# Optimization experiments

Measured on AMD Instinct MI355X. Metric: run time of the kernel, lower is better.

The kernel has to match this reference:

```python
import jax, jax.numpy as jnp
import numpy as np

B, S, D, H = 4, 2048, 1024, 16
HD = D // H  # head dim = 64


def setup_inputs() -> dict:
    key = jax.random.key(0)
    ks = jax.random.split(key, 5)
    scale = 0.02
    return {
        "x": jax.random.normal(ks[0], (B, S, D), dtype=jnp.float32),
        "w_qkv": jax.random.normal(ks[1], (D, 3 * D), dtype=jnp.float32) * scale,
        "b_qkv": jax.random.normal(ks[2], (3 * D,), dtype=jnp.float32) * scale,
        "w_proj": jax.random.normal(ks[3], (D, D), dtype=jnp.float32) * scale,
        "b_proj": jax.random.normal(ks[4], (D,), dtype=jnp.float32) * scale,
    }


def reference(x, w_qkv, b_qkv, w_proj, b_proj):
    # Fused QKV projection: [B,S,D] @ [D,3D] -> [B,S,3D]
    qkv = jnp.einsum('bsd,de->bse', x, w_qkv) + b_qkv
    q, k, v = jnp.split(qkv, 3, axis=-1)
    # [B,S,D] -> [B,H,S,hd]
    def heads(t):
        return t.reshape(B, S, H, HD).transpose(0, 2, 1, 3)
    q, k, v = heads(q), heads(k), heads(v)
    # Scaled dot-product attention (non-causal, matching torch SDPA defaults)
    scores = jnp.einsum('bhsd,bhtd->bhst', q, k) / jnp.sqrt(jnp.float32(HD))
    attn = jax.nn.softmax(scores, axis=-1)
    out = jnp.einsum('bhst,bhtd->bhsd', attn, v)
    # [B,H,S,hd] -> [B,S,D]
    out = out.transpose(0, 2, 1, 3).reshape(B, S, D)
    return jnp.einsum('bsd,de->bse', out, w_proj) + b_proj
```

## Files before the change

kernel.cpp:

```cpp
#include <hip/hip_runtime.h>
#include <hip/hip_bf16.h>
#include <cstdint>

typedef __attribute__((ext_vector_type(8))) __bf16 bf16x8;
typedef __attribute__((ext_vector_type(4))) __bf16 bf16x4;
typedef __attribute__((ext_vector_type(4))) float f32x4;

#define MFMA16(a, b, c) __builtin_amdgcn_mfma_f32_16x16x32_bf16(a, b, c, 0, 0, 0)

static constexpr float SCQ = 0.18033688f;

__device__ __forceinline__ void gload16(const void* g, void* l) {
  __builtin_amdgcn_global_load_lds(
      (const __attribute__((address_space(1))) void*)g,
      (__attribute__((address_space(3))) void*)l, 16, 0, 0);
}

__global__ __launch_bounds__(256) void conv_x(const float* __restrict__ in,
                                              __bf16* __restrict__ out) {
  const size_t i = ((size_t)blockIdx.x * 256 + threadIdx.x) * 8;
  const float4 v0 = *(const float4*)(in + i);
  const float4 v1 = *(const float4*)(in + i + 4);
  bf16x8 o = {(__bf16)v0.x, (__bf16)v0.y, (__bf16)v0.z, (__bf16)v0.w,
              (__bf16)v1.x, (__bf16)v1.y, (__bf16)v1.z, (__bf16)v1.w};
  *(bf16x8*)(out + i) = o;
}

__global__ __launch_bounds__(256) void conv_wt(const float* __restrict__ W,
                                               __bf16* __restrict__ Wt,
                                               int K, int N) {
  __shared__ float tile[64][65];
  const int nb = blockIdx.x * 64, kb = blockIdx.y * 64;
  const int t = threadIdx.x, tr = t >> 4, tc = t & 15;
  #pragma unroll
  for (int p = 0; p < 4; ++p) {
    const float4 v =
        *(const float4*)(W + (size_t)(kb + p * 16 + tr) * N + nb + tc * 4);
    tile[p * 16 + tr][tc * 4 + 0] = v.x;
    tile[p * 16 + tr][tc * 4 + 1] = v.y;
    tile[p * 16 + tr][tc * 4 + 2] = v.z;
    tile[p * 16 + tr][tc * 4 + 3] = v.w;
  }
  __syncthreads();
  #pragma unroll
  for (int p = 0; p < 4; ++p) {
    const int n = p * 16 + tr, kk = tc * 4;
    bf16x4 o = {(__bf16)tile[kk + 0][n], (__bf16)tile[kk + 1][n],
                (__bf16)tile[kk + 2][n], (__bf16)tile[kk + 3][n]};
    *(bf16x4*)(Wt + (size_t)(nb + n) * K + kb + kk) = o;
  }
}

__global__ __launch_bounds__(256) void qkv_gemm_b(
    const __bf16* __restrict__ A, const __bf16* __restrict__ Bt,
    const float* __restrict__ bias,
    __bf16* __restrict__ Qb, __bf16* __restrict__ Kb, __bf16* __restrict__ Vt)
{
  __shared__ alignas(16) __bf16 a_sh[128 * 32];
  __shared__ alignas(16) __bf16 b_sh[128 * 32];
  const int id = blockIdx.x;
  const int wg = (id & 7) * 192 + (id >> 3);
  const int n0 = (wg % 24) * 128, m0 = (wg / 24) * 128;
  const int t = threadIdx.x, wave = t >> 6, lane = t & 63;
  const int r = lane & 15, g = lane >> 4;
  const int wm = (wave >> 1) * 64, wn = (wave & 1) * 64;
  f32x4 acc[4][4] = {};

  const int srow = wave * 16 + (lane >> 2);
  const int scol = (lane & 3) * 8;
  const __bf16* gA = A + (size_t)(m0 + srow) * 1024 + scol;
  const __bf16* gB = Bt + (size_t)(n0 + srow) * 1024 + scol;
  __bf16* lA = a_sh + wave * 512;
  __bf16* lB = b_sh + wave * 512;

  for (int k0 = 0; k0 < 1024; k0 += 32) {
    __syncthreads();
    gload16(gA + k0, lA);
    gload16(gA + 64 * 1024 + k0, lA + 2048);
    gload16(gB + k0, lB);
    gload16(gB + 64 * 1024 + k0, lB + 2048);
    __syncthreads();
    bf16x8 af[4], bfr[4];
    #pragma unroll
    for (int i = 0; i < 4; ++i)
      af[i] = *(bf16x8*)&a_sh[(wm + i * 16 + r) * 32 + g * 8];
    #pragma unroll
    for (int j = 0; j < 4; ++j)
      bfr[j] = *(bf16x8*)&b_sh[(wn + j * 16 + r) * 32 + g * 8];
    #pragma unroll
    for (int i = 0; i < 4; ++i)
      #pragma unroll
      for (int j = 0; j < 4; ++j)
        acc[i][j] = MFMA16(af[i], bfr[j], acc[i][j]);
  }

  const int which = n0 >> 10;
  const int bb = m0 >> 11;
  const int sbase = (m0 & 2047) + wm;
  #pragma unroll
  for (int j = 0; j < 4; ++j) {
    const int nc = n0 + wn + j * 16 + r;
    const float bv = bias[nc];
    const int hh = (nc & 1023) >> 6;
    const int d = nc & 63;
    #pragma unroll
    for (int i = 0; i < 4; ++i) {
      const int ss0 = sbase + i * 16 + g * 4;
      if (which == 0) {
        #pragma unroll
        for (int rr = 0; rr < 4; ++rr)
          Qb[((size_t)(bb * 16 + hh) * 2048 + ss0 + rr) * 64 + d] =
              (__bf16)((acc[i][j][rr] + bv) * SCQ);
      } else if (which == 1) {
        #pragma unroll
        for (int rr = 0; rr < 4; ++rr)
          Kb[((size_t)(bb * 16 + hh) * 2048 + ss0 + rr) * 64 +
             (d ^ ((((ss0 + rr) & 7)) << 3))] =
              (__bf16)(acc[i][j][rr] + bv);
      } else {
        bf16x4 vv;
        #pragma unroll
        for (int rr = 0; rr < 4; ++rr) vv[rr] = (__bf16)(acc[i][j][rr] + bv);
        const int v5 = ss0 & 31;
        const int pcol = (ss0 & ~31) + 8 * ((v5 >> 2) & 3) + 4 * (v5 >> 4);
        const int scol2 = (pcol & ~127) | ((pcol & 127) ^ ((d & 7) << 3));
        *(bf16x4*)&Vt[((size_t)(bb * 16 + hh) * 64 + d) * 2048 + scol2] = vv;
      }
    }
  }
}

__global__ __launch_bounds__(256) void proj_gemm_b(
    const __bf16* __restrict__ A, const __bf16* __restrict__ Bt,
    const float* __restrict__ bias, float* __restrict__ out)
{
  __shared__ alignas(16) __bf16 a_sh[128 * 32];
  __shared__ alignas(16) __bf16 b_sh[128 * 32];
  const int id = blockIdx.x;
  const int wg = (id & 7) * 64 + (id >> 3);
  const int n0 = (wg & 7) * 128, m0 = (wg >> 3) * 128;
  const int t = threadIdx.x, wave = t >> 6, lane = t & 63;
  const int r = lane & 15, g = lane >> 4;
  const int wm = (wave >> 1) * 64, wn = (wave & 1) * 64;
  f32x4 acc[4][4] = {};

  const int srow = wave * 16 + (lane >> 2);
  const int scol = (lane & 3) * 8;
  const __bf16* gA = A + (size_t)(m0 + srow) * 1024 + scol;
  const __bf16* gB = Bt + (size_t)(n0 + srow) * 1024 + scol;
  __bf16* lA = a_sh + wave * 512;
  __bf16* lB = b_sh + wave * 512;

  for (int k0 = 0; k0 < 1024; k0 += 32) {
    __syncthreads();
    gload16(gA + k0, lA);
    gload16(gA + 64 * 1024 + k0, lA + 2048);
    gload16(gB + k0, lB);
    gload16(gB + 64 * 1024 + k0, lB + 2048);
    __syncthreads();
    bf16x8 af[4], bfr[4];
    #pragma unroll
    for (int i = 0; i < 4; ++i)
      af[i] = *(bf16x8*)&a_sh[(wm + i * 16 + r) * 32 + g * 8];
    #pragma unroll
    for (int j = 0; j < 4; ++j)
      bfr[j] = *(bf16x8*)&b_sh[(wn + j * 16 + r) * 32 + g * 8];
    #pragma unroll
    for (int i = 0; i < 4; ++i)
      #pragma unroll
      for (int j = 0; j < 4; ++j)
        acc[i][j] = MFMA16(af[i], bfr[j], acc[i][j]);
  }

  #pragma unroll
  for (int j = 0; j < 4; ++j) {
    const int nc = n0 + wn + j * 16 + r;
    const float bv = bias[nc];
    #pragma unroll
    for (int i = 0; i < 4; ++i)
      #pragma unroll
      for (int rr = 0; rr < 4; ++rr)
        out[(size_t)(m0 + wm + i * 16 + g * 4 + rr) * 1024 + nc] =
            acc[i][j][rr] + bv;
  }
}

__global__ __launch_bounds__(256, 4) void attn_kernel(
    const __bf16* __restrict__ Q, const __bf16* __restrict__ K,
    const __bf16* __restrict__ Vt, __bf16* __restrict__ AO)
{
  __shared__ alignas(16) char lds[2][16384];

  const int p = blockIdx.x;
  const int hd = (p & 7) + 8 * (p >> 7);
  const int qt = (p >> 3) & 15;
  const int b = hd >> 4, h = hd & 15;

  const int t = threadIdx.x, wave = t >> 6, lane = t & 63;
  const int r = lane & 15, g = lane >> 4;

  const __bf16* Qp = Q + (size_t)hd * (2048 * 64);
  const char* Kh = (const char*)(K + (size_t)hd * (2048 * 64));
  const char* Vh = (const char*)(Vt + (size_t)hd * (64 * 2048));
  const int q0 = qt * 128 + wave * 32;

  bf16x8 qf[2][2];
  #pragma unroll
  for (int qh = 0; qh < 2; ++qh)
    #pragma unroll
    for (int hh = 0; hh < 2; ++hh)
      qf[qh][hh] =
          *(const bf16x8*)(Qp + (size_t)(q0 + qh * 16 + r) * 64 + hh * 32 + g * 8);

  float mrun[2] = {0.f, 0.f};
  float lrun[2] = {0.f, 0.f};
  f32x4 o[4][2] = {};

  const int lofs0 = wave * 1024;
  const int gofs0 = wave * 1024 + lane * 16;

  #define STAGE(t32, bi)                                                  \
    {                                                                     \
      char* lb = lds[bi];                                                 \
      _Pragma("unroll")                                                   \
      for (int rnd = 0; rnd < 2; ++rnd) {                                 \
        const int fb = rnd * 4096 + gofs0;                                \
        gload16(Kh + (size_t)(t32) * 8192 + fb, lb + rnd * 4096 + lofs0); \
        gload16(Vh + (size_t)(fb >> 7) * 4096 + (size_t)(t32) * 128 +     \
                    (fb & 127),                                           \
                lb + 8192 + rnd * 4096 + lofs0);                          \
      }                                                                   \
    }

  STAGE(0, 0);
  __syncthreads();

  const int sw = (r & 7) << 4;

  for (int t32 = 0; t32 < 32; ++t32) {
    const int cur = t32 & 1;
    if (t32 < 31) STAGE(t32 + 1, cur ^ 1);

    const char* kb = lds[cur];
    const char* vb = lds[cur] + 8192;

    f32x4 sacc[4][2];
    const f32x4 seed0 = {-mrun[0], -mrun[0], -mrun[0], -mrun[0]};
    const f32x4 seed1 = {-mrun[1], -mrun[1], -mrun[1], -mrun[1]};
    __builtin_amdgcn_s_setprio(1);
    #pragma unroll
    for (int kt = 0; kt < 4; ++kt) {
      const int rowb = (kt * 16 + r) * 128;
      const bf16x8 kf0 = *(const bf16x8*)(kb + rowb + ((16 * g) ^ sw));
      const bf16x8 kf1 = *(const bf16x8*)(kb + rowb + ((64 + 16 * g) ^ sw));
      f32x4 s0 = MFMA16(kf0, qf[0][0], seed0);
      s0 = MFMA16(kf1, qf[0][1], s0);
      sacc[kt][0] = s0;
      f32x4 s1 = MFMA16(kf0, qf[1][0], seed1);
      s1 = MFMA16(kf1, qf[1][1], s1);
      sacc[kt][1] = s1;
    }
    __builtin_amdgcn_s_setprio(0);

    bf16x8 pf[2][2];
    #pragma unroll
    for (int qh = 0; qh < 2; ++qh) {
      float a0 = fmaxf(fmaxf(sacc[0][qh][0], sacc[0][qh][1]),
                       fmaxf(sacc[0][qh][2], sacc[0][qh][3]));
      float a1 = fmaxf(fmaxf(sacc[1][qh][0], sacc[1][qh][1]),
                       fmaxf(sacc[1][qh][2], sacc[1][qh][3]));
      float a2 = fmaxf(fmaxf(sacc[2][qh][0], sacc[2][qh][1]),
                       fmaxf(sacc[2][qh][2], sacc[2][qh][3]));
      float a3 = fmaxf(fmaxf(sacc[3][qh][0], sacc[3][qh][1]),
                       fmaxf(sacc[3][qh][2], sacc[3][qh][3]));
      const float tm = fmaxf(fmaxf(a0, a1), fmaxf(a2, a3));

      float s = 0.f;
      if (__any(tm > 6.0f)) {
        float rm = fmaxf(tm, __shfl_xor(tm, 16));
        rm = fmaxf(rm, __shfl_xor(rm, 32));
        const float dl = fmaxf(rm, 0.f);
        const float al = exp2f(-dl);
        mrun[qh] += dl;
        #pragma unroll
        for (int kt = 0; kt < 4; ++kt)
          #pragma unroll
          for (int rr = 0; rr < 4; ++rr) {
            const float e = exp2f(sacc[kt][qh][rr] - dl);
            s += e;
            pf[qh][kt >> 1][(kt & 1) * 4 + rr] = (__bf16)e;
          }
        lrun[qh] = lrun[qh] * al + s;
        #pragma unroll
        for (int dt = 0; dt < 4; ++dt)
          #pragma unroll
          for (int rr = 0; rr < 4; ++rr)
            o[dt][qh][rr] *= al;
      } else {
        #pragma unroll
        for (int kt = 0; kt < 4; ++kt)
          #pragma unroll
          for (int rr = 0; rr < 4; ++rr) {
            const float e = exp2f(sacc[kt][qh][rr]);
            s += e;
            pf[qh][kt >> 1][(kt & 1) * 4 + rr] = (__bf16)e;
          }
        lrun[qh] += s;
      }
    }

    __builtin_amdgcn_s_setprio(1);
    #pragma unroll
    for (int c = 0; c < 2; ++c)
      #pragma unroll
      for (int dt = 0; dt < 4; ++dt) {
        const bf16x8 vf = *(const bf16x8*)(vb + (dt * 16 + r) * 128 +
                                           ((c * 64 + 16 * g) ^ sw));
        o[dt][0] = MFMA16(vf, pf[0][c], o[dt][0]);
        o[dt][1] = MFMA16(vf, pf[1][c], o[dt][1]);
      }
    __builtin_amdgcn_s_setprio(0);

    __syncthreads();
  }
  #undef STAGE

  #pragma unroll
  for (int qh = 0; qh < 2; ++qh) {
    float lr = lrun[qh];
    lr += __shfl_xor(lr, 16);
    lr += __shfl_xor(lr, 32);
    const float inv = 1.0f / lr;
    const int ss = q0 + qh * 16 + r;
    #pragma unroll
    for (int dt = 0; dt < 4; ++dt) {
      bf16x4 ov;
      #pragma unroll
      for (int rr = 0; rr < 4; ++rr)
        ov[rr] = (__bf16)(o[dt][qh][rr] * inv);
      *(bf16x4*)&AO[((size_t)b * 2048 + ss) * 1024 + h * 64 + dt * 16 + 4 * g] = ov;
    }
  }
}

extern "C" void kernel_launch(void* const* d_in, const int* in_sizes, int n_in,
                              void* d_out, int out_size, void* d_ws, size_t ws_size,
                              hipStream_t stream) {
  (void)in_sizes; (void)n_in; (void)out_size; (void)ws_size;
  const float* x      = (const float*)d_in[0];
  const float* w_qkv  = (const float*)d_in[1];
  const float* b_qkv  = (const float*)d_in[2];
  const float* w_proj = (const float*)d_in[3];
  const float* b_proj = (const float*)d_in[4];
  float* out = (float*)d_out;

  char* ws = (char*)d_ws;
  const size_t E2 = (size_t)8192 * 1024 * 2;
  __bf16* Qb  = (__bf16*)(ws);
  __bf16* Kb  = (__bf16*)(ws + E2);
  __bf16* Vt  = (__bf16*)(ws + 2 * E2);
  __bf16* Xb  = (__bf16*)(ws + 3 * E2);
  __bf16* AO  = Xb;
  __bf16* Wqt = (__bf16*)(ws + 4 * E2);
  __bf16* Wpt = (__bf16*)(ws + 4 * E2 + (size_t)3072 * 1024 * 2);

  conv_x<<<4096, 256, 0, stream>>>(x, Xb);
  conv_wt<<<dim3(48, 16), 256, 0, stream>>>(w_qkv, Wqt, 1024, 3072);
  conv_wt<<<dim3(16, 16), 256, 0, stream>>>(w_proj, Wpt, 1024, 1024);
  qkv_gemm_b<<<1536, 256, 0, stream>>>(Xb, Wqt, b_qkv, Qb, Kb, Vt);
  attn_kernel<<<1024, 256, 0, stream>>>(Qb, Kb, Vt, AO);
  proj_gemm_b<<<512, 256, 0, stream>>>(AO, Wpt, b_proj, out);
}
```

Before: 245.6 us.

## Replace GEMMs with 128x256-tile, 8-wave, triple-buffered pipelined kernel

The two separate QKV and projection GEMM kernels become one templated kernel that uses 128x256 tiles, 512 threads and a K-step of 64. Global-to-LDS loads are triple-buffered with prefetch two steps ahead, and a XOR swizzle avoids LDS bank conflicts. MFMA phases are split with s_setprio and explicit barriers so memory latency overlaps with compute. The large LDS footprint (144KB) limits occupancy to one block per CU, and the projection grid shrinks to 256 blocks, which may underfill the GPU.

Result: no change. 241.3 us (-1.8%).

```diff
diff --git a/kernel.cpp b/kernel.cpp
--- a/kernel.cpp
+++ b/kernel.cpp
@@ -51,137 +51,170 @@
   }
 }
 
-__global__ __launch_bounds__(256) void qkv_gemm_b(
+template <int MODE>
+__global__ __launch_bounds__(512) void gemm_t4(
     const __bf16* __restrict__ A, const __bf16* __restrict__ Bt,
     const float* __restrict__ bias,
-    __bf16* __restrict__ Qb, __bf16* __restrict__ Kb, __bf16* __restrict__ Vt)
+    __bf16* __restrict__ Qb, __bf16* __restrict__ Kb, __bf16* __restrict__ Vt,
+    float* __restrict__ outF)
 {
-  __shared__ alignas(16) __bf16 a_sh[128 * 32];
-  __shared__ alignas(16) __bf16 b_sh[128 * 32];
+  __shared__ alignas(16) char lds_[3 * 49152];
+
   const int id = blockIdx.x;
-  const int wg = (id & 7) * 192 + (id >> 3);
-  const int n0 = (wg % 24) * 128, m0 = (wg / 24) * 128;
-  const int t = threadIdx.x, wave = t >> 6, lane = t & 63;
+  constexpr int NB = (MODE == 0) ? 12 : 4;
+  constexpr int CH = (MODE == 0) ? 96 : 32;
+  const int wg = (id & 7) * CH + (id >> 3);
+  const int m0 = (wg / NB) * 128;
+  const int n0 = (wg % NB) * 256;
+
+  const int t = threadIdx.x, w = t >> 6, lane = t & 63;
   const int r = lane & 15, g = lane >> 4;
-  const int wm = (wave >> 1) * 64, wn = (wave & 1) * 64;
+  const int wr = w >> 2, wc = w & 3;
+
+  const char* Ac = (const char*)A + (size_t)m0 * 2048;
+  const char* Bc = (const char*)Bt + (size_t)n0 * 2048;
+
+  #define STAGE(kt_)                                                       \
+    {                                                                      \
+      char* lb = lds_ + ((kt_) % 3) * 49152;                               \
+      _Pragma("unroll")                                                    \
+      for (int rnd = 0; rnd < 2; ++rnd) {                                  \
+        const int c = rnd * 512 + t;                                       \
+        const int row = c >> 3;                                            \
+        const int kc = (c & 7) ^ (row & 7);                                \
+        gload16(Ac + (size_t)row * 2048 + (kt_) * 128 + kc * 16,           \
+                lb + rnd * 8192 + t * 16);                                 \
+      }                                                                    \
+      _Pragma("unroll")                                                    \
+      for (int rnd = 0; rnd < 4; ++rnd) {                                  \
+        const int c = rnd * 512 + t;                                       \
+        const int row = c >> 3;                                            \
+        const int kc = (c & 7) ^ (row & 7);                                \
+        gload16(Bc + (size_t)row * 2048 + (kt_) * 128 + kc * 16,           \
+                lb + 16384 + rnd * 8192 + t * 16);                         \
+      }                                                                    \
+    }
+
   f32x4 acc[4][4] = {};
-
-  const int srow = wave * 16 + (lane >> 2);
-  const int scol = (lane & 3) * 8;
-  const __bf16* gA = A + (size_t)(m0 + srow) * 1024 + scol;
-  const __bf16* gB = Bt + (size_t)(n0 + srow) * 1024 + scol;
-  __bf16* lA = a_sh + wave * 512;
-  __bf16* lB = b_sh + wave * 512;
-
-  for (int k0 = 0; k0 < 1024; k0 += 32) {
-    __syncthreads();
-    gload16(gA + k0, lA);
-    gload16(gA + 64 * 1024 + k0, lA + 2048);
-    gload16(gB + k0, lB);
-    gload16(gB + 64 * 1024 + k0, lB + 2048);
-    __syncthreads();
-    bf16x8 af[4], bfr[4];
+  const int sw = (r & 7) << 4;
+
+  STAGE(0);
+  STAGE(1);
+  asm volatile("s_waitcnt vmcnt(6)" ::: "memory");
+  __builtin_amdgcn_sched_barrier(0);
+  __builtin_amdgcn_s_barrier();
+  __builtin_amdgcn_sched_barrier(0);
+
+  for (int kt = 0; kt < 16; ++kt) {
+    if (kt < 14) STAGE(kt + 2);
+    const char* lb = lds_ + (kt % 3) * 49152;
+
+    bf16x8 af[4][2], bf0[2][2];
     #pragma unroll
     for (int i = 0; i < 4; ++i)
-      af[i] = *(bf16x8*)&a_sh[(wm + i * 16 + r) * 32 + g * 8];
-    #pragma unroll
-    for (int j = 0; j < 4; ++j)
-      bfr[j] = *(bf16x8*)&b_sh[(wn + j * 16 + r) * 32 + g * 8];
-    #pragma unroll
-    for (int i = 0; i < 4; ++i)
-      #pragma unroll
-      for (int j = 0; j < 4; ++j)
-        acc[i][j] = MFMA16(af[i], bfr[j], acc[i][j]);
-  }
-
-  const int which = n0 >> 10;
-  const int bb = m0 >> 11;
-  const int sbase = (m0 & 2047) + wm;
-  #pragma unroll
-  for (int j = 0; j < 4; ++j) {
-    const int nc = n0 + wn + j * 16 + r;
-    const float bv = bias[nc];
-    const int hh = (nc & 1023) >> 6;
-    const int d = nc & 63;
-    #pragma unroll
-    for (int i = 0; i < 4; ++i) {
-      const int ss0 = sbase + i * 16 + g * 4;
-      if (which == 0) {
+      #pragma unroll
+      for (int kk = 0; kk < 2; ++kk)
+        af[i][kk] = *(const bf16x8*)(lb + (wr * 64 + i * 16 + r) * 128 +
+                                     ((kk * 64 + g * 16) ^ sw));
+    #pragma unroll
+    for (int jj = 0; jj < 2; ++jj)
+      #pragma unroll
+      for (int kk = 0; kk < 2; ++kk)
+        bf0[jj][kk] = *(const bf16x8*)(lb + 16384 +
+                                       (wc * 64 + jj * 16 + r) * 128 +
+                                       ((kk * 64 + g * 16) ^ sw));
+    asm volatile("s_waitcnt lgkmcnt(0)" ::: "memory");
+    __builtin_amdgcn_sched_barrier(0);
+    __builtin_amdgcn_s_setprio(1);
+    #pragma unroll
+    for (int kk = 0; kk < 2; ++kk)
+      #pragma unroll
+      for (int i = 0; i < 4; ++i)
+        #pragma unroll
+        for (int jj = 0; jj < 2; ++jj)
+          acc[i][jj] = MFMA16(af[i][kk], bf0[jj][kk], acc[i][jj]);
+    __builtin_amdgcn_s_setprio(0);
+    __builtin_amdgcn_s_barrier();
+    __builtin_amdgcn_sched_barrier(0);
+
+    bf16x8 bf1[2][2];
+    #pragma unroll
+    for (int jj = 0; jj < 2; ++jj)
+      #pragma unroll
+      for (int kk = 0; kk < 2; ++kk)
+        bf1[jj][kk] = *(const bf16x8*)(lb + 16384 +
+                                       (wc * 64 + (2 + jj) * 16 + r) * 128 +
+                                       ((kk * 64 + g * 16) ^ sw));
+    asm volatile("s_waitcnt lgkmcnt(0)" ::: "memory");
+    __builtin_amdgcn_sched_barrier(0);
+    __builtin_amdgcn_s_setprio(1);
+    #pragma unroll
+    for (int kk = 0; kk < 2; ++kk)
+      #pragma unroll
+      for (int i = 0; i < 4; ++i)
+        #pragma unroll
+        for (int jj = 0; jj < 2; ++jj)
+          acc[i][2 + jj] = MFMA16(af[i][kk], bf1[jj][kk], acc[i][2 + jj]);
+    __builtin_amdgcn_s_setprio(0);
+
+    if (kt < 14) {
+      asm volatile("s_waitcnt vmcnt(6)" ::: "memory");
+    } else {
+      asm volatile("s_waitcnt vmcnt(0)" ::: "memory");
+    }
+    __builtin_amdgcn_sched_barrier(0);
+    __builtin_amdgcn_s_barrier();
+    __builtin_amdgcn_sched_barrier(0);
+  }
+  #undef STAGE
+
+  if (MODE == 0) {
+    const int which = n0 >> 10;
+    const int bb = m0 >> 11;
+    const int sbase = (m0 & 2047) + wr * 64;
+    #pragma unroll
+    for (int j = 0; j < 4; ++j) {
+      const int nc = n0 + wc * 64 + j * 16 + r;
+      const float bv = bias[nc];
+      const int hh = (nc & 1023) >> 6;
+      const int d = nc & 63;
+      #pragma unroll
+      for (int i = 0; i < 4; ++i) {
+        const int ss0 = sbase + i * 16 + g * 4;
+        if (which == 0) {
+          #pragma unroll
+          for (int rr = 0; rr < 4; ++rr)
+            Qb[((size_t)(bb * 16 + hh) * 2048 + ss0 + rr) * 64 + d] =
+                (__bf16)((acc[i][j][rr] + bv) * SCQ);
+        } else if (which == 1) {
+          #pragma unroll
+          for (int rr = 0; rr < 4; ++rr)
+            Kb[((size_t)(bb * 16 + hh) * 2048 + ss0 + rr) * 64 +
+               (d ^ ((((ss0 + rr) & 7)) << 3))] =
+                (__bf16)(acc[i][j][rr] + bv);
+        } else {
+          bf16x4 vv;
+          #pragma unroll
+          for (int rr = 0; rr < 4; ++rr) vv[rr] = (__bf16)(acc[i][j][rr] + bv);
+          const int v5 = ss0 & 31;
+          const int pcol = (ss0 & ~31) + 8 * ((v5 >> 2) & 3) + 4 * (v5 >> 4);
+          const int scol2 = (pcol & ~127) | ((pcol & 127) ^ ((d & 7) << 3));
+          *(bf16x4*)&Vt[((size_t)(bb * 16 + hh) * 64 + d) * 2048 + scol2] = vv;
+        }
+      }
+    }
+  } else {
+    #pragma unroll
+    for (int j = 0; j < 4; ++j) {
+      const int nc = n0 + wc * 64 + j * 16 + r;
+      const float bv = bias[nc];
+      #pragma unroll
+      for (int i = 0; i < 4; ++i)
         #pragma unroll
         for (int rr = 0; rr < 4; ++rr)
-          Qb[((size_t)(bb * 16 + hh) * 2048 + ss0 + rr) * 64 + d] =
-              (__bf16)((acc[i][j][rr] + bv) * SCQ);
-      } else if (which == 1) {
-        #pragma unroll
-        for (int rr = 0; rr < 4; ++rr)
-          Kb[((size_t)(bb * 16 + hh) * 2048 + ss0 + rr) * 64 +
-             (d ^ ((((ss0 + rr) & 7)) << 3))] =
-              (__bf16)(acc[i][j][rr] + bv);
-      } else {
-        bf16x4 vv;
-        #pragma unroll
-        for (int rr = 0; rr < 4; ++rr) vv[rr] = (__bf16)(acc[i][j][rr] + bv);
-        const int v5 = ss0 & 31;
-        const int pcol = (ss0 & ~31) + 8 * ((v5 >> 2) & 3) + 4 * (v5 >> 4);
-        const int scol2 = (pcol & ~127) | ((pcol & 127) ^ ((d & 7) << 3));
-        *(bf16x4*)&Vt[((size_t)(bb * 16 + hh) * 64 + d) * 2048 + scol2] = vv;
-      }
-    }
-  }
-}
-
-__global__ __launch_bounds__(256) void proj_gemm_b(
-    const __bf16* __restrict__ A, const __bf16* __restrict__ Bt,
-    const float* __restrict__ bias, float* __restrict__ out)
-{
-  __shared__ alignas(16) __bf16 a_sh[128 * 32];
-  __shared__ alignas(16) __bf16 b_sh[128 * 32];
-  const int id = blockIdx.x;
-  const int wg = (id & 7) * 64 + (id >> 3);
-  const int n0 = (wg & 7) * 128, m0 = (wg >> 3) * 128;
-  const int t = threadIdx.x, wave = t >> 6, lane = t & 63;
-  const int r = lane & 15, g = lane >> 4;
-  const int wm = (wave >> 1) * 64, wn = (wave & 1) * 64;
-  f32x4 acc[4][4] = {};
-
-  const int srow = wave * 16 + (lane >> 2);
-  const int scol = (lane & 3) * 8;
-  const __bf16* gA = A + (size_t)(m0 + srow) * 1024 + scol;
-  const __bf16* gB = Bt + (size_t)(n0 + srow) * 1024 + scol;
-  __bf16* lA = a_sh + wave * 512;
-  __bf16* lB = b_sh + wave * 512;
-
-  for (int k0 = 0; k0 < 1024; k0 += 32) {
-    __syncthreads();
-    gload16(gA + k0, lA);
-    gload16(gA + 64 * 1024 + k0, lA + 2048);
-    gload16(gB + k0, lB);
-    gload16(gB + 64 * 1024 + k0, lB + 2048);
-    __syncthreads();
-    bf16x8 af[4], bfr[4];
-    #pragma unroll
-    for (int i = 0; i < 4; ++i)
-      af[i] = *(bf16x8*)&a_sh[(wm + i * 16 + r) * 32 + g * 8];
-    #pragma unroll
-    for (int j = 0; j < 4; ++j)
-      bfr[j] = *(bf16x8*)&b_sh[(wn + j * 16 + r) * 32 + g * 8];
-    #pragma unroll
-    for (int i = 0; i < 4; ++i)
-      #pragma unroll
-      for (int j = 0; j < 4; ++j)
-        acc[i][j] = MFMA16(af[i], bfr[j], acc[i][j]);
-  }
-
-  #pragma unroll
-  for (int j = 0; j < 4; ++j) {
-    const int nc = n0 + wn + j * 16 + r;
-    const float bv = bias[nc];
-    #pragma unroll
-    for (int i = 0; i < 4; ++i)
-      #pragma unroll
-      for (int rr = 0; rr < 4; ++rr)
-        out[(size_t)(m0 + wm + i * 16 + g * 4 + rr) * 1024 + nc] =
-            acc[i][j][rr] + bv;
+          outF[(size_t)(m0 + wr * 64 + i * 16 + g * 4 + rr) * 1024 + nc] =
+              acc[i][j][rr] + bv;
+    }
   }
 }
 
@@ -367,7 +400,8 @@
   conv_x<<<4096, 256, 0, stream>>>(x, Xb);
   conv_wt<<<dim3(48, 16), 256, 0, stream>>>(w_qkv, Wqt, 1024, 3072);
   conv_wt<<<dim3(16, 16), 256, 0, stream>>>(w_proj, Wpt, 1024, 1024);
-  qkv_gemm_b<<<1536, 256, 0, stream>>>(Xb, Wqt, b_qkv, Qb, Kb, Vt);
+  gemm_t4<0><<<768, 512, 0, stream>>>(Xb, Wqt, b_qkv, Qb, Kb, Vt, nullptr);
   attn_kernel<<<1024, 256, 0, stream>>>(Qb, Kb, Vt, AO);
-  proj_gemm_b<<<512, 256, 0, stream>>>(AO, Wpt, b_proj, out);
-}
+  gemm_t4<1><<<256, 512, 0, stream>>>(AO, Wpt, b_proj, nullptr, nullptr,
+                                      nullptr, out);
+}
```
